# Optimization experiments

Measured on AMD Instinct MI355X. Metric: run time of the kernel, lower is better.

Reference implementation:

```python
import jax, jax.numpy as jnp
import numpy as np

N_NODES = 100000
N_EDGES = 1600000
IN_FEATS = 256
OUT_FEATS = 32
NUM_HEADS = 4
EW_DIMS = 2
NEG_SLOPE = 0.2


def setup_inputs() -> dict:
    key = jax.random.key(0)
    ks = jax.random.split(key, 8)
    feat = jax.random.normal(ks[0], (N_NODES, IN_FEATS), dtype=jnp.float32)
    e_w = jax.random.normal(ks[1], (N_EDGES, NUM_HEADS, EW_DIMS), dtype=jnp.float32)
    src = jax.random.randint(ks[2], (N_EDGES,), 0, N_NODES, dtype=jnp.int32)
    dst = jax.random.randint(ks[3], (N_EDGES,), 0, N_NODES, dtype=jnp.int32)
    # Params (xavier-like scale)
    W_fc = jax.random.normal(ks[4], (NUM_HEADS * OUT_FEATS, IN_FEATS), dtype=jnp.float32) * (2.0 / (IN_FEATS + NUM_HEADS * OUT_FEATS)) ** 0.5
    attn_l = jax.random.normal(ks[5], (1, NUM_HEADS, OUT_FEATS), dtype=jnp.float32) * 0.1
    attn_r = jax.random.normal(ks[6], (1, NUM_HEADS, OUT_FEATS), dtype=jnp.float32) * 0.1
    attn_ew = jax.random.normal(ks[7], (1, NUM_HEADS, EW_DIMS), dtype=jnp.float32) * 0.1
    return {"feat": feat, "e_w": e_w, "src": src, "dst": dst,
            "W_fc": W_fc, "attn_l": attn_l, "attn_r": attn_r, "attn_ew": attn_ew}


def reference(feat, e_w, src, dst, W_fc, attn_l, attn_r, attn_ew):
    N = feat.shape[0]
    # Dense projection: [N, H, F]
    feat_src = (feat @ W_fc.T).reshape(N, NUM_HEADS, OUT_FEATS)
    # Per-node attention logits: [N, H]
    el = jnp.sum(feat_src * attn_l, axis=-1)
    er = jnp.sum(feat_src * attn_r, axis=-1)
    # Edge additive attention (u_add_v) + edge-feature term: [E, H]
    e = el[src] + er[dst] + jnp.sum(e_w * attn_ew, axis=-1)
    e = jnp.where(e > 0, e, NEG_SLOPE * e)  # LeakyReLU
    # Edge softmax over incoming edges per dst node (numerically stable)
    e_max = jax.ops.segment_max(e, dst, num_segments=N)  # [N, H]
    e_exp = jnp.exp(e - e_max[dst])
    denom = jax.ops.segment_sum(e_exp, dst, num_segments=N)  # [N, H]
    a = e_exp / denom[dst]  # [E, H]
    # Weighted scatter-sum aggregation (u_mul_e + sum): [N, H, F]
    msgs = feat_src[src] * a[:, :, None]
    rst = jax.ops.segment_sum(msgs, dst, num_segments=N)
    # ELU activation
    return jax.nn.elu(rst)
```

## Files before the change

### kernel.cpp

```cpp
#include <hip/hip_runtime.h>
#include <hip/hip_fp16.h>

#define N_NODES 100000
#define N_EDGES 1600000
#define IN_F 256
#define OUT_F 32
#define HEADS 4
#define HF 128
#define NEG_SLOPE 0.2f

#define EPB 4096
#define NBLK ((N_EDGES + EPB - 1) / EPB)
#define NBIN ((N_NODES + 255) / 256)

typedef _Float16 f16;
typedef __attribute__((ext_vector_type(2))) _Float16 f16x2;
typedef __attribute__((ext_vector_type(8))) _Float16 f16x8;
typedef __attribute__((ext_vector_type(2))) __fp16 hf16x2;
typedef __attribute__((ext_vector_type(4))) float f32x4;
typedef __attribute__((ext_vector_type(2))) float f32x2;
typedef __attribute__((ext_vector_type(4))) int i32x4;

__device__ __forceinline__ unsigned pack_h2(float a, float b) {
    return (unsigned)__half_as_ushort(__float2half_rn(a)) |
           ((unsigned)__half_as_ushort(__float2half_rn(b)) << 16);
}
__device__ __forceinline__ float unpack_lo(unsigned u) {
    return __half2float(__ushort_as_half((ushort)(u & 0xFFFFu)));
}
__device__ __forceinline__ float unpack_hi(unsigned u) {
    return __half2float(__ushort_as_half((ushort)(u >> 16)));
}

__global__ void wconv_kernel(const float* __restrict__ W, f16* __restrict__ Wh) {
    const int i = blockIdx.x * blockDim.x + threadIdx.x;
    if (i < HF * IN_F) Wh[i] = (f16)W[i];
}

__global__ __launch_bounds__(256) void gemm2(const float* __restrict__ feat,
                                             const f16* __restrict__ Wh,
                                             f16* __restrict__ fsh) {
    extern __shared__ char smem[];
    const int t = threadIdx.x;
#pragma unroll
    for (int i = 0; i < 16; ++i) {
        const int c = t + i * 256;
        const int row = c >> 5;
        const int cb = (c & 31) << 4;
        const i32x4 v = __builtin_nontemporal_load((const i32x4*)((const char*)Wh + (size_t)c * 16));
        *(i32x4*)(smem + row * 512 + (cb ^ ((row & 7) << 4))) = v;
    }
    __syncthreads();

    const int w = t >> 6, l = t & 63;
    const int lr = l & 15, lk = l >> 4;
    const int base = blockIdx.x * 128 + w * 32;

    f32x4 acc[2][8];
#pragma unroll
    for (int m = 0; m < 2; ++m)
#pragma unroll
        for (int ot = 0; ot < 8; ++ot) acc[m][ot] = (f32x4){0.f, 0.f, 0.f, 0.f};

    int r0 = base + lr;
    int r1 = base + 16 + lr;
    r0 = r0 < N_NODES ? r0 : N_NODES - 1;
    r1 = r1 < N_NODES ? r1 : N_NODES - 1;
    const float* p0 = feat + (size_t)r0 * IN_F + lk * 8;
    const float* p1 = feat + (size_t)r1 * IN_F + lk * 8;

#pragma unroll
    for (int kc = 0; kc < 8; ++kc) {
        f16x8 a[2];
        {
            const f32x4 x0 = __builtin_nontemporal_load((const f32x4*)(p0 + kc * 32));
            const f32x4 x1 = __builtin_nontemporal_load((const f32x4*)(p0 + kc * 32 + 4));
            union { f16x8 v; hf16x2 p[4]; } ua;
            ua.p[0] = __builtin_amdgcn_cvt_pkrtz(x0.x, x0.y);
            ua.p[1] = __builtin_amdgcn_cvt_pkrtz(x0.z, x0.w);
            ua.p[2] = __builtin_amdgcn_cvt_pkrtz(x1.x, x1.y);
            ua.p[3] = __builtin_amdgcn_cvt_pkrtz(x1.z, x1.w);
            a[0] = ua.v;
        }
        {
            const f32x4 x0 = __builtin_nontemporal_load((const f32x4*)(p1 + kc * 32));
            const f32x4 x1 = __builtin_nontemporal_load((const f32x4*)(p1 + kc * 32 + 4));
            union { f16x8 v; hf16x2 p[4]; } ua;
            ua.p[0] = __builtin_amdgcn_cvt_pkrtz(x0.x, x0.y);
            ua.p[1] = __builtin_amdgcn_cvt_pkrtz(x0.z, x0.w);
            ua.p[2] = __builtin_amdgcn_cvt_pkrtz(x1.x, x1.y);
            ua.p[3] = __builtin_amdgcn_cvt_pkrtz(x1.z, x1.w);
            a[1] = ua.v;
        }
#pragma unroll
        for (int ot = 0; ot < 8; ++ot) {
            const int row = ot * 16 + lr;
            const f16x8 b = *(const f16x8*)(smem + row * 512 +
                                            ((kc * 64 + lk * 16) ^ ((lr & 7) << 4)));
            acc[0][ot] = __builtin_amdgcn_mfma_f32_16x16x32_f16(a[0], b, acc[0][ot], 0, 0, 0);
            acc[1][ot] = __builtin_amdgcn_mfma_f32_16x16x32_f16(a[1], b, acc[1][ot], 0, 0, 0);
        }
    }
#pragma unroll
    for (int m = 0; m < 2; ++m)
#pragma unroll
        for (int reg = 0; reg < 4; ++reg) {
            const int n = base + m * 16 + lk * 4 + reg;
            if (n < N_NODES) {
#pragma unroll
                for (int ot = 0; ot < 8; ++ot)
                    fsh[(size_t)n * HF + ot * 16 + lr] = (f16)acc[m][ot][reg];
            }
        }
}

__global__ void elr_kernel(const f16* __restrict__ fsh,
                           const float* __restrict__ attn_l,
                           const float* __restrict__ attn_r,
                           float* __restrict__ el, float* __restrict__ er) {
    const int tid = blockIdx.x * blockDim.x + threadIdx.x;
    if (tid >= N_NODES * HEADS) return;
    const int h = tid & 3, n = tid >> 2;
    const f16* p = fsh + (size_t)n * HF + h * OUT_F;
    float sl = 0.f, sr = 0.f;
#pragma unroll
    for (int f = 0; f < OUT_F; f += 8) {
        const f16x8 v8 = *(const f16x8*)(p + f);
#pragma unroll
        for (int j = 0; j < 8; ++j) {
            const float v = (float)v8[j];
            sl += v * attn_l[h * OUT_F + f + j];
            sr += v * attn_r[h * OUT_F + f + j];
        }
    }
    el[tid] = sl;
    er[tid] = sr;
}

__global__ __launch_bounds__(512) void count_kernel(const int* __restrict__ dst,
                                                    int* __restrict__ blockcnt) {
    __shared__ int bins[NBIN];
    const int bid = blockIdx.x, t = threadIdx.x;
    for (int i = t; i < NBIN; i += 512) bins[i] = 0;
    __syncthreads();
    const int base = bid * EPB;
#pragma unroll
    for (int k = 0; k < 8; ++k) {
        const int e = base + t + k * 512;
        if (e < N_EDGES) atomicAdd(&bins[dst[e] >> 8], 1);
    }
    __syncthreads();
    for (int i = t; i < NBIN; i += 512) blockcnt[bid * NBIN + i] = bins[i];
}

__global__ __launch_bounds__(512) void colscan_kernel(const int* __restrict__ blockcnt,
                                                      int* __restrict__ blockpfx,
                                                      int* __restrict__ total) {
    __shared__ int sh[512];
    const int b = blockIdx.x, t = threadIdx.x;
    const int v = (t < NBLK) ? blockcnt[t * NBIN + b] : 0;
    sh[t] = v;
    __syncthreads();
    for (int off = 1; off < 512; off <<= 1) {
        const int x = (t >= off) ? sh[t - off] : 0;
        __syncthreads();
        sh[t] += x;
        __syncthreads();
    }
    if (t < NBLK) blockpfx[b * NBLK + t] = sh[t] - v;
    if (t == 511) total[b] = sh[t];
}

__global__ __launch_bounds__(512) void binscan_kernel(const int* __restrict__ total,
                                                      int* __restrict__ binbase) {
    __shared__ int sh[512];
    const int t = threadIdx.x;
    const int v = (t < NBIN) ? total[t] : 0;
    sh[t] = v;
    __syncthreads();
    for (int off = 1; off < 512; off <<= 1) {
        const int x = (t >= off) ? sh[t - off] : 0;
        __syncthreads();
        sh[t] += x;
        __syncthreads();
    }
    if (t < NBIN) binbase[t] = sh[t] - v;
    if (t == NBIN - 1) binbase[NBIN] = sh[t];
}

__global__ __launch_bounds__(512) void binscat_kernel(const int* __restrict__ src,
                                                      const int* __restrict__ dst,
                                                      const float* __restrict__ e_w,
                                                      const float* __restrict__ attn_ew,
                                                      const int* __restrict__ binbase,
                                                      const int* __restrict__ blockpfx,
                                                      int4* __restrict__ recs) {
    __shared__ int cur[NBIN];
    const int bid = blockIdx.x, t = threadIdx.x;
    for (int i = t; i < NBIN; i += 512) cur[i] = binbase[i] + blockpfx[i * NBLK + bid];
    __syncthreads();
    const float4 a01 = *(const float4*)(attn_ew);
    const float4 a23 = *(const float4*)(attn_ew + 4);
    const int base = bid * EPB;
#pragma unroll
    for (int k = 0; k < 8; ++k) {
        const int e = base + t + k * 512;
        if (e < N_EDGES) {
            const int s = __builtin_nontemporal_load(src + e);
            const int d = __builtin_nontemporal_load(dst + e);
            const f32x4 w01 = __builtin_nontemporal_load((const f32x4*)(e_w + (size_t)e * 8));
            const f32x4 w23 = __builtin_nontemporal_load((const f32x4*)(e_w + (size_t)e * 8 + 4));
            const float d0 = w01.x * a01.x + w01.y * a01.y;
            const float d1 = w01.z * a01.z + w01.w * a01.w;
            const float d2 = w23.x * a23.x + w23.y * a23.y;
            const float d3 = w23.z * a23.z + w23.w * a23.w;
            const int pos = atomicAdd(&cur[d >> 8], 1);
            int4 r;
            r.x = s; r.y = d;
            r.z = (int)pack_h2(d0, d1);
            r.w = (int)pack_h2(d2, d3);
            recs[pos] = r;
        }
    }
}

__global__ __launch_bounds__(512) void finalize_kernel(const int* __restrict__ binbase,
                                                       const float* __restrict__ el,
                                                       int4* __restrict__ recs,
                                                       int* __restrict__ offs,
                                                       int* __restrict__ cnt) {
    __shared__ int lcnt[256];
    __shared__ int sh[512];
    __shared__ int loff[256], lcur[256];
    const int b = blockIdx.x, t = threadIdx.x;
    const int n0 = b << 8;
    const int beg = binbase[b], end = binbase[b + 1];
    const int m = end - beg;
    if (t < 256) lcnt[t] = 0;
    __syncthreads();
    int4 r[10];
#pragma unroll
    for (int k = 0; k < 10; ++k) {
        const int i = t + k * 512;
        if (i < m) {
            r[k] = recs[beg + i];
            atomicAdd(&lcnt[r[k].y - n0], 1);
        }
    }
    __syncthreads();
    {
        const int v = (t < 256) ? lcnt[t] : 0;
        sh[t] = v;
        __syncthreads();
        for (int off = 1; off < 256; off <<= 1) {
            const int x = (t >= off) ? sh[t - off] : 0;
            __syncthreads();
            sh[t] += x;
            __syncthreads();
        }
        if (t < 256) { loff[t] = sh[t] - v; lcur[t] = sh[t] - v; }
    }
    __syncthreads();
#pragma unroll
    for (int k = 0; k < 10; ++k) {
        const int i = t + k * 512;
        if (i < m) {
            const int4 rec = r[k];
            const float4 l4 = *(const float4*)(el + (size_t)rec.x * 4);
            const float v0 = l4.x + unpack_lo((unsigned)rec.z);
            const float v1 = l4.y + unpack_hi((unsigned)rec.z);
            const float v2 = l4.z + unpack_lo((unsigned)rec.w);
            const float v3 = l4.w + unpack_hi((unsigned)rec.w);
            const int slot = atomicAdd(&lcur[rec.y - n0], 1);
            int4 fr;
            fr.x = rec.x;
            fr.y = (int)pack_h2(v0, v1);
            fr.z = (int)pack_h2(v2, v3);
            fr.w = 0;
            recs[beg + slot] = fr;
        }
    }
    if (t < 256 && n0 + t < N_NODES) {
        offs[n0 + t] = beg + loff[t];
        cnt[n0 + t]  = lcnt[t];
    }
}

#define CH 64
__global__ __launch_bounds__(64) void agg_kernel(const int* __restrict__ offs,
                                                 const int* __restrict__ cnt,
                                                 const int4* __restrict__ recs,
                                                 const float* __restrict__ er,
                                                 const f16* __restrict__ fsh,
                                                 float* __restrict__ out) {
    __shared__ float sh_w[CH * 4];
    __shared__ int   sh_src[CH];
    const int n  = blockIdx.x;
    const int t  = threadIdx.x;
    const int eh = t >> 5;
    const int q  = t & 31;
    const int h  = q >> 3;
    const int beg = offs[n];
    const int deg = cnt[n];
    const float4 ern = *(const float4*)(er + (size_t)n * 4);

    float den = 0.f;
    float a0 = 0.f, a1 = 0.f, a2 = 0.f, a3 = 0.f;

    for (int c = 0; c < deg; c += CH) {
        const int cn = min(CH, deg - c);
        if (t < cn) {
            const i32x4 r = __builtin_nontemporal_load((const i32x4*)recs + (beg + c + t));
            float v0 = unpack_lo((unsigned)r.y) + ern.x;
            float v1 = unpack_hi((unsigned)r.y) + ern.y;
            float v2 = unpack_lo((unsigned)r.z) + ern.z;
            float v3 = unpack_hi((unsigned)r.z) + ern.w;
            v0 = v0 > 0.f ? v0 : NEG_SLOPE * v0;
            v1 = v1 > 0.f ? v1 : NEG_SLOPE * v1;
            v2 = v2 > 0.f ? v2 : NEG_SLOPE * v2;
            v3 = v3 > 0.f ? v3 : NEG_SLOPE * v3;
            *(float4*)&sh_w[t * 4] = make_float4(__expf(v0), __expf(v1),
                                                 __expf(v2), __expf(v3));
            sh_src[t] = r.x;
        } else {
            *(float4*)&sh_w[t * 4] = make_float4(0.f, 0.f, 0.f, 0.f);
            sh_src[t] = 0;
        }
        __syncthreads();
#pragma unroll 4
        for (int j = 0; j < cn; j += 2) {
            const int je = j + eh;
            const float wgt = sh_w[je * 4 + h];
            const int s = sh_src[je];
            union { uint2 u; f16x2 p[2]; } g;
            g.u = *(const uint2*)(fsh + (size_t)s * HF + q * 4);
            a0 += (float)g.p[0][0] * wgt;
            a1 += (float)g.p[0][1] * wgt;
            a2 += (float)g.p[1][0] * wgt;
            a3 += (float)g.p[1][1] * wgt;
            den += wgt;
        }
        __syncthreads();
    }
    a0 += __shfl_xor(a0, 32);
    a1 += __shfl_xor(a1, 32);
    a2 += __shfl_xor(a2, 32);
    a3 += __shfl_xor(a3, 32);
    den += __shfl_xor(den, 32);
    if (t < 32) {
        const float inv = (deg > 0) ? 1.f / den : 0.f;
        float r0 = a0 * inv, r1 = a1 * inv, r2 = a2 * inv, r3 = a3 * inv;
        r0 = r0 > 0.f ? r0 : expm1f(r0);
        r1 = r1 > 0.f ? r1 : expm1f(r1);
        r2 = r2 > 0.f ? r2 : expm1f(r2);
        r3 = r3 > 0.f ? r3 : expm1f(r3);
        const f32x4 o4 = { r0, r1, r2, r3 };
        __builtin_nontemporal_store(o4, (f32x4*)(out + (size_t)n * HF + t * 4));
    }
}

static size_t align16(size_t x) { return (x + 15) & ~(size_t)15; }

extern "C" void kernel_launch(void* const* d_in, const int* in_sizes, int n_in,
                              void* d_out, int out_size, void* d_ws, size_t ws_size,
                              hipStream_t stream) {
    const float* feat    = (const float*)d_in[0];
    const float* e_w     = (const float*)d_in[1];
    const int*   src     = (const int*)d_in[2];
    const int*   dst     = (const int*)d_in[3];
    const float* W       = (const float*)d_in[4];
    const float* attn_l  = (const float*)d_in[5];
    const float* attn_r  = (const float*)d_in[6];
    const float* attn_ew = (const float*)d_in[7];
    float* out = (float*)d_out;

    char* p = (char*)d_ws;
    f16*    fsh      = (f16*)p;     p += align16((size_t)N_NODES * HF * 2);
    float*  el       = (float*)p;   p += align16((size_t)N_NODES * HEADS * 4);
    float*  er       = (float*)p;   p += align16((size_t)N_NODES * HEADS * 4);
    int*    offs     = (int*)p;     p += align16((size_t)N_NODES * 4);
    int*    cnt      = (int*)p;     p += align16((size_t)N_NODES * 4);
    f16*    Wh       = (f16*)p;     p += align16((size_t)HF * IN_F * 2);
    int*    blockcnt = (int*)p;     p += align16((size_t)NBLK * NBIN * 4);
    int*    blockpfx = (int*)p;     p += align16((size_t)NBIN * NBLK * 4);
    int*    total    = (int*)p;     p += align16((size_t)NBIN * 4);
    int*    binbase  = (int*)p;     p += align16((size_t)(NBIN + 1) * 4);
    int4*   recs     = (int4*)p;    p += align16((size_t)N_EDGES * 16);

    wconv_kernel<<<(HF * IN_F + 255) / 256, 256, 0, stream>>>(W, Wh);
    gemm2<<<(N_NODES + 127) / 128, 256, 65536, stream>>>(feat, Wh, fsh);
    elr_kernel<<<(N_NODES * HEADS + 255) / 256, 256, 0, stream>>>(fsh, attn_l, attn_r, el, er);
    count_kernel<<<NBLK, 512, 0, stream>>>(dst, blockcnt);
    colscan_kernel<<<NBIN, 512, 0, stream>>>(blockcnt, blockpfx, total);
    binscan_kernel<<<1, 512, 0, stream>>>(total, binbase);
    binscat_kernel<<<NBLK, 512, 0, stream>>>(src, dst, e_w, attn_ew, binbase, blockpfx, recs);
    finalize_kernel<<<NBIN, 512, 0, stream>>>(binbase, el, recs, offs, cnt);
    agg_kernel<<<N_NODES, 64, 0, stream>>>(offs, cnt, recs, er, fsh, out);
}
```

Measured before the change: 215.5 us.

## Process eight edges per wavefront iteration with 16-half loads per lane

The aggregation kernel now assigns 8 lanes per edge, each loading 32 bytes (16 fp16 features), so a wavefront handles 8 edges at once instead of 2. Weight and source index are packed together in shared memory, so each lane needs one LDS read. The goal is more memory-level parallelism on the gathers and fewer loop iterations per node. The cost is 16 accumulators per lane, a three-step cross-lane reduction, and more wasted lanes when a chunk holds few edges.

Result: slower. 247.9 us (+15.0%).

```diff
diff --git a/kernel.cpp b/kernel.cpp
--- a/kernel.cpp
+++ b/kernel.cpp
@@ -293,19 +293,20 @@
                                                  const float* __restrict__ er,
                                                  const f16* __restrict__ fsh,
                                                  float* __restrict__ out) {
-    __shared__ float sh_w[CH * 4];
-    __shared__ int   sh_src[CH];
+    __shared__ uint2 sh_ws[CH * 4];
     const int n  = blockIdx.x;
     const int t  = threadIdx.x;
-    const int eh = t >> 5;
-    const int q  = t & 31;
-    const int h  = q >> 3;
+    const int eh = t >> 3;
+    const int q  = t & 7;
+    const int h  = q >> 1;
     const int beg = offs[n];
     const int deg = cnt[n];
     const float4 ern = *(const float4*)(er + (size_t)n * 4);
 
     float den = 0.f;
-    float a0 = 0.f, a1 = 0.f, a2 = 0.f, a3 = 0.f;
+    f32x4 acc[4];
+#pragma unroll
+    for (int i = 0; i < 4; ++i) acc[i] = (f32x4){0.f, 0.f, 0.f, 0.f};
 
     for (int c = 0; c < deg; c += CH) {
         const int cn = min(CH, deg - c);
@@ -319,43 +320,74 @@
             v1 = v1 > 0.f ? v1 : NEG_SLOPE * v1;
             v2 = v2 > 0.f ? v2 : NEG_SLOPE * v2;
             v3 = v3 > 0.f ? v3 : NEG_SLOPE * v3;
-            *(float4*)&sh_w[t * 4] = make_float4(__expf(v0), __expf(v1),
-                                                 __expf(v2), __expf(v3));
-            sh_src[t] = r.x;
+            const unsigned s = (unsigned)r.x;
+            sh_ws[t * 4 + 0] = make_uint2(__float_as_uint(__expf(v0)), s);
+            sh_ws[t * 4 + 1] = make_uint2(__float_as_uint(__expf(v1)), s);
+            sh_ws[t * 4 + 2] = make_uint2(__float_as_uint(__expf(v2)), s);
+            sh_ws[t * 4 + 3] = make_uint2(__float_as_uint(__expf(v3)), s);
         } else {
-            *(float4*)&sh_w[t * 4] = make_float4(0.f, 0.f, 0.f, 0.f);
-            sh_src[t] = 0;
-        }
-        __syncthreads();
-#pragma unroll 4
-        for (int j = 0; j < cn; j += 2) {
+            const uint2 z = make_uint2(0u, 0u);
+            sh_ws[t * 4 + 0] = z;
+            sh_ws[t * 4 + 1] = z;
+            sh_ws[t * 4 + 2] = z;
+            sh_ws[t * 4 + 3] = z;
+        }
+        __syncthreads();
+#pragma unroll 2
+        for (int j = 0; j < cn; j += 8) {
             const int je = j + eh;
-            const float wgt = sh_w[je * 4 + h];
-            const int s = sh_src[je];
-            union { uint2 u; f16x2 p[2]; } g;
-            g.u = *(const uint2*)(fsh + (size_t)s * HF + q * 4);
-            a0 += (float)g.p[0][0] * wgt;
-            a1 += (float)g.p[0][1] * wgt;
-            a2 += (float)g.p[1][0] * wgt;
-            a3 += (float)g.p[1][1] * wgt;
+            const uint2 ws = sh_ws[je * 4 + h];
+            const float wgt = __uint_as_float(ws.x);
+            const f16* gp = fsh + ((size_t)ws.y * HF + q * 16);
+            union { i32x4 u; f16x2 p[4]; } g0, g1;
+            g0.u = *(const i32x4*)gp;
+            g1.u = *(const i32x4*)(gp + 8);
+            acc[0][0] += (float)g0.p[0][0] * wgt;
+            acc[0][1] += (float)g0.p[0][1] * wgt;
+            acc[0][2] += (float)g0.p[1][0] * wgt;
+            acc[0][3] += (float)g0.p[1][1] * wgt;
+            acc[1][0] += (float)g0.p[2][0] * wgt;
+            acc[1][1] += (float)g0.p[2][1] * wgt;
+            acc[1][2] += (float)g0.p[3][0] * wgt;
+            acc[1][3] += (float)g0.p[3][1] * wgt;
+            acc[2][0] += (float)g1.p[0][0] * wgt;
+            acc[2][1] += (float)g1.p[0][1] * wgt;
+            acc[2][2] += (float)g1.p[1][0] * wgt;
+            acc[2][3] += (float)g1.p[1][1] * wgt;
+            acc[3][0] += (float)g1.p[2][0] * wgt;
+            acc[3][1] += (float)g1.p[2][1] * wgt;
+            acc[3][2] += (float)g1.p[3][0] * wgt;
+            acc[3][3] += (float)g1.p[3][1] * wgt;
             den += wgt;
         }
         __syncthreads();
     }
-    a0 += __shfl_xor(a0, 32);
-    a1 += __shfl_xor(a1, 32);
-    a2 += __shfl_xor(a2, 32);
-    a3 += __shfl_xor(a3, 32);
+#pragma unroll
+    for (int i = 0; i < 4; ++i)
+#pragma unroll
+        for (int k = 0; k < 4; ++k) {
+            float a = acc[i][k];
+            a += __shfl_xor(a, 8);
+            a += __shfl_xor(a, 16);
+            a += __shfl_xor(a, 32);
+            acc[i][k] = a;
+        }
+    den += __shfl_xor(den, 8);
+    den += __shfl_xor(den, 16);
     den += __shfl_xor(den, 32);
-    if (t < 32) {
+    if (t < 8) {
         const float inv = (deg > 0) ? 1.f / den : 0.f;
-        float r0 = a0 * inv, r1 = a1 * inv, r2 = a2 * inv, r3 = a3 * inv;
-        r0 = r0 > 0.f ? r0 : expm1f(r0);
-        r1 = r1 > 0.f ? r1 : expm1f(r1);
-        r2 = r2 > 0.f ? r2 : expm1f(r2);
-        r3 = r3 > 0.f ? r3 : expm1f(r3);
-        const f32x4 o4 = { r0, r1, r2, r3 };
-        __builtin_nontemporal_store(o4, (f32x4*)(out + (size_t)n * HF + t * 4));
+        float* op = out + (size_t)n * HF + q * 16;
+#pragma unroll
+        for (int i = 0; i < 4; ++i) {
+            f32x4 o;
+#pragma unroll
+            for (int k = 0; k < 4; ++k) {
+                float r = acc[i][k] * inv;
+                o[k] = r > 0.f ? r : expm1f(r);
+            }
+            __builtin_nontemporal_store(o, (f32x4*)(op + i * 4));
+        }
     }
 }
 
```
